# Kernel optimization log

Measured on AMD Instinct MI355X. Metric: run time of the kernel, lower is better.

## Reference

```python
import jax, jax.numpy as jnp
import numpy as np

VOCAB = 50257
EXTRA = 64          # static over-approximation of num_oovs
SEQ = 1024
T_DEC = 100
E = 128
H = 160             # encoder hidden per direction; decoder hidden = 2H = 320
UNK = 3
START = 0
NEG = -1e9


def lstm_cell(x, h, c, wih, whh, bih, bhh):
    # torch gate order: i, f, g, o
    g = x @ wih.T + h @ whh.T + bih + bhh
    i, f, gg, o = jnp.split(g, 4, axis=-1)
    c = jax.nn.sigmoid(f) * c + jax.nn.sigmoid(i) * jnp.tanh(gg)
    h = jax.nn.sigmoid(o) * jnp.tanh(c)
    return h, c


def run_lstm(xs, wih, whh, bih, bhh, hdim):
    def step(carry, x):
        h, c = carry
        h, c = lstm_cell(x, h, c, wih, whh, bih, bhh)
        return (h, c), h
    init = (jnp.zeros((hdim,), xs.dtype), jnp.zeros((hdim,), xs.dtype))
    (hf, _), hs = jax.lax.scan(step, init, xs)
    return hs, hf


def setup_inputs() -> dict:
    key = jax.random.key(0)
    ks = jax.random.split(key, 20)
    rn = lambda k, shape, s: (jax.random.normal(k, shape, dtype=jnp.float32) * s)
    inp = {
        'input_ids': jax.random.randint(ks[0], (SEQ,), 0, VOCAB + EXTRA),
        'embedding': rn(ks[1], (VOCAB, E), 0.1),
        'enc_wih_f': rn(ks[2], (4 * H, E), 0.08),
        'enc_whh_f': rn(ks[3], (4 * H, H), 0.08),
        'enc_bih_f': rn(ks[4], (4 * H,), 0.05),
        'enc_bhh_f': rn(ks[5], (4 * H,), 0.05),
        'enc_wih_b': rn(ks[6], (4 * H, E), 0.08),
        'enc_whh_b': rn(ks[7], (4 * H, H), 0.08),
        'enc_bih_b': rn(ks[8], (4 * H,), 0.05),
        'enc_bhh_b': rn(ks[9], (4 * H,), 0.05),
        'dec_wih': rn(ks[10], (8 * H, E), 0.08),
        'dec_whh': rn(ks[11], (8 * H, 2 * H), 0.08),
        'dec_bih': rn(ks[12], (8 * H,), 0.05),
        'dec_bhh': rn(ks[13], (8 * H,), 0.05),
        'enc_attn_proj': rn(ks[14], (2 * H, 2 * H), 0.02),
        'dec_attn_proj': rn(ks[15], (2 * H, 2 * H), 0.02),
        'vocab_proj': rn(ks[16], (E, 6 * H), 0.05),
        'out_bias': rn(ks[17], (VOCAB,), 0.01),
        'switch_w': rn(ks[18], (1, 6 * H), 0.05),
        'switch_b': rn(ks[19], (1,), 0.05),
    }
    return inp


def reference(input_ids, embedding, enc_wih_f, enc_whh_f, enc_bih_f, enc_bhh_f,
              enc_wih_b, enc_whh_b, enc_bih_b, enc_bhh_b,
              dec_wih, dec_whh, dec_bih, dec_bhh,
              enc_attn_proj, dec_attn_proj, vocab_proj, out_bias,
              switch_w, switch_b):
    ids_in = jnp.where(input_ids >= VOCAB, UNK, input_ids)
    emb = embedding[ids_in]                               # [S, E]

    # bidirectional encoder LSTM
    h_fwd, hfin_f = run_lstm(emb, enc_wih_f, enc_whh_f, enc_bih_f, enc_bhh_f, H)
    h_bwd_rev, hfin_b = run_lstm(emb[::-1], enc_wih_b, enc_whh_b, enc_bih_b, enc_bhh_b, H)
    enc_h = jnp.concatenate([h_fwd, h_bwd_rev[::-1]], axis=-1)   # [S, 2H]

    # step-invariant vocab projection: tanh(W_emb @ vocab_proj) -> [V, 6H]
    out_proj = jnp.tanh(embedding @ vocab_proj)

    # precompute projected encoder states for attention: [S, 2H]
    enc_proj_h = enc_h @ enc_attn_proj.T

    h0 = jnp.concatenate([hfin_f, hfin_b])                # [2H]
    c0 = jnp.zeros((2 * H,), enc_h.dtype)
    dec_buf0 = jnp.zeros((T_DEC, 2 * H), enc_h.dtype)
    cum0 = jnp.zeros((SEQ,), enc_h.dtype)
    tok0 = jnp.asarray(START, dtype=input_ids.dtype)
    t_range = jnp.arange(T_DEC)

    def step(carry, t):
        h, c, cum, dec_buf, tok = carry
        x = embedding[jnp.where(tok >= VOCAB, UNK, tok)]
        h, c = lstm_cell(x, h, c, dec_wih, dec_whh, dec_bih, dec_bhh)

        # intra-temporal encoder attention
        scores = enc_proj_h @ h                           # [S] = h @ W_e @ enc_h.T
        cum_safe = jnp.where(t == 0, 1.0, cum)
        temporal = jnp.where(t == 0, scores, jnp.exp(scores) / cum_safe)
        attn = jax.nn.softmax(temporal)
        enc_ctx = attn @ enc_h                            # [2H]

        # intra-decoder attention over previous decoder hidden states
        dscores = (h @ dec_attn_proj) @ dec_buf.T         # [T_DEC]
        dmask = t_range < t
        dattn = jax.nn.softmax(jnp.where(dmask, dscores, NEG))
        dec_ctx = jnp.where(t == 0, jnp.zeros_like(h), dattn @ dec_buf)

        concat = jnp.concatenate([h, enc_ctx, dec_ctx])   # [6H]
        vocab_dist = jax.nn.softmax(out_proj @ concat + out_bias)  # [V]
        p_copy = jax.nn.sigmoid(jnp.dot(switch_w[0], concat) + switch_b[0])
        gen = jnp.pad((1.0 - p_copy) * vocab_dist, (0, EXTRA))     # [V+EXTRA]
        final = gen.at[input_ids].add(p_copy * attn)      # pointer scatter-add

        cum = cum + scores
        dec_buf = dec_buf.at[t].set(h)
        tok = jnp.argmax(final).astype(input_ids.dtype)   # greedy decode
        return (h, c, cum, dec_buf, tok), final

    _, finals = jax.lax.scan(step, (h0, c0, cum0, dec_buf0, tok0), t_range)
    return finals                                         # [T_DEC, V+EXTRA]
```

## Files before the change

kernel.cpp:

```cpp
#include <hip/hip_runtime.h>
#include <cstdint>

#define VOCAB 50257
#define VTOT  50321
#define TDEC  100
#define UNK   3
#define NBLK  256
#define NTHR  512
#define VPB   256
#define VPAD  50304

static const size_t OFF_EMB    = 0;
static const size_t OFF_WIHT_F = 131072;
static const size_t OFF_WIHT_B = 212992;
static const size_t OFF_WTE    = 294912;
static const size_t OFF_XG     = 397312;
static const size_t OFF_ENCH   = 1708032;
static const size_t OFF_EPH    = 2035712;
static const size_t OFF_DECBUF = 2363392;
static const size_t OFF_GATES  = 2395392;
static const size_t OFF_HPAR   = 2396672;
static const size_t OFF_CPAR   = 2399232;
static const size_t OFF_DCTX   = 2404352;
static const size_t OFF_H0     = 2404672;
static const size_t OFF_TEMP   = 2404992;
static const size_t OFF_ATTN   = 2406016;
static const size_t OFF_PMS    = 2407040;
static const size_t OFF_BM     = 2407552;
static const size_t OFF_BS     = 2407808;
static const size_t OFF_AVAL   = 2408064;
static const size_t OFF_AIDX   = 2408320;
static const size_t OFF_BAR    = 2408576;
static const size_t OFF_SKEY   = 2408640;
static const size_t OFF_SPOS   = 2409664;
static const size_t OFF_BSTART = 2410688;
static const size_t OFF_WT     = 2411008;

__device__ __forceinline__ float sigmf(float x) { return 1.f / (1.f + expf(-x)); }

__device__ __forceinline__ float wsum64(float x) {
#pragma unroll
  for (int m = 1; m < 64; m <<= 1) x += __shfl_xor(x, m, 64);
  return x;
}

__device__ __forceinline__ unsigned short bf16r(float x) {
  uint32_t b = __float_as_uint(x);
  uint32_t r = (b + 0x7fffu + ((b >> 16) & 1u)) >> 16;
  return (unsigned short)r;
}

__device__ __forceinline__ float cload(const float* p) {
  return __hip_atomic_load((float*)p, __ATOMIC_RELAXED, __HIP_MEMORY_SCOPE_AGENT);
}
__device__ __forceinline__ void cstore(float* p, float v) {
  __hip_atomic_store(p, v, __ATOMIC_RELAXED, __HIP_MEMORY_SCOPE_AGENT);
}
__device__ __forceinline__ int cloadi(const int* p) {
  return __hip_atomic_load((int*)p, __ATOMIC_RELAXED, __HIP_MEMORY_SCOPE_AGENT);
}
__device__ __forceinline__ void cstorei(int* p, int v) {
  __hip_atomic_store(p, v, __ATOMIC_RELAXED, __HIP_MEMORY_SCOPE_AGENT);
}

__device__ __forceinline__ void gridbar(float* ws) {
  int* bar = (int*)(ws + OFF_BAR);
  __syncthreads();
  if (threadIdx.x == 0) {
    asm volatile("s_waitcnt vmcnt(0) lgkmcnt(0)" ::: "memory");
    int g = __hip_atomic_load(&bar[32], __ATOMIC_RELAXED, __HIP_MEMORY_SCOPE_AGENT);
    int old = __hip_atomic_fetch_add(&bar[0], 1, __ATOMIC_RELAXED, __HIP_MEMORY_SCOPE_AGENT);
    if (old == NBLK - 1) {
      __hip_atomic_store(&bar[0], 0, __ATOMIC_RELAXED, __HIP_MEMORY_SCOPE_AGENT);
      __hip_atomic_store(&bar[32], g + 1, __ATOMIC_RELAXED, __HIP_MEMORY_SCOPE_AGENT);
    } else {
      while (__hip_atomic_load(&bar[32], __ATOMIC_RELAXED, __HIP_MEMORY_SCOPE_AGENT) == g)
        __builtin_amdgcn_s_sleep(2);
    }
  }
  __syncthreads();
}

__global__ __launch_bounds__(256) void k_setup(float* __restrict__ ws, const int* __restrict__ ids,
                                               const float* __restrict__ embt, const float* __restrict__ ewf,
                                               const float* __restrict__ ewb, const float* __restrict__ eap) {
  int idx = blockIdx.x * 256 + threadIdx.x;
  if (idx < 131072) {
    int tt = idx >> 7, e = idx & 127;
    int id = ids[tt]; if (id >= VOCAB) id = UNK;
    ws[OFF_EMB + idx] = embt[(size_t)id * 128 + e];
  } else if (idx < 212992) {
    int i = idx - 131072;
    int k = i / 640, g = i - (i / 640) * 640;
    ws[OFF_WIHT_F + i] = ewf[(size_t)g * 128 + k];
  } else if (idx < 294912) {
    int i = idx - 212992;
    int k = i / 640, g = i - (i / 640) * 640;
    ws[OFF_WIHT_B + i] = ewb[(size_t)g * 128 + k];
  } else if (idx < 397312) {
    int i = idx - 294912;
    int k = i / 320, j = i - (i / 320) * 320;
    ws[OFF_WTE + i] = eap[(size_t)j * 320 + k];
  }
}

__global__ __launch_bounds__(256) void k_xg(float* __restrict__ ws,
                                            const float* __restrict__ bif, const float* __restrict__ bhf,
                                            const float* __restrict__ bib, const float* __restrict__ bhb) {
  int idx = blockIdx.x * 256 + threadIdx.x;
  int d = idx / 655360;
  int r = idx - d * 655360;
  int tt = r / 640, g = r - (r / 640) * 640;
  const float* wT = ws + (d ? OFF_WIHT_B : OFF_WIHT_F);
  const float* er = ws + OFF_EMB + (size_t)(d ? (1023 - tt) : tt) * 128;
  float acc = d ? (bib[g] + bhb[g]) : (bif[g] + bhf[g]);
#pragma unroll 4
  for (int k = 0; k < 128; ++k) acc += er[k] * wT[(size_t)k * 640 + g];
  ws[OFF_XG + idx] = acc;
}

__global__ __launch_bounds__(256) void k_outproj(const float* __restrict__ embt, const float* __restrict__ vp,
                                                 float* __restrict__ ws) {
  __shared__ float As[64][128];
  __shared__ float Bs[128][64];
  __shared__ unsigned T[32][64];
  const int tid = threadIdx.x;
  const int v0 = blockIdx.x * 64, n0 = blockIdx.y * 64;
  for (int c = 0; c < 32; ++c) {
    int idx = c * 256 + tid;
    int m = idx >> 7, k = idx & 127;
    int v = v0 + m;
    As[m][k] = (v < VOCAB) ? embt[(size_t)v * 128 + k] : 0.f;
    int k2 = idx >> 6, n = idx & 63;
    Bs[k2][n] = vp[(size_t)k2 * 960 + n0 + n];
  }
  __syncthreads();
  const int mi = tid >> 4, ni = tid & 15;
  float acc[4][4] = {};
  for (int k = 0; k < 128; ++k) {
    float a0 = As[mi * 4 + 0][k], a1 = As[mi * 4 + 1][k], a2 = As[mi * 4 + 2][k], a3 = As[mi * 4 + 3][k];
    float4 b = *(const float4*)&Bs[k][ni * 4];
    acc[0][0] += a0 * b.x; acc[0][1] += a0 * b.y; acc[0][2] += a0 * b.z; acc[0][3] += a0 * b.w;
    acc[1][0] += a1 * b.x; acc[1][1] += a1 * b.y; acc[1][2] += a1 * b.z; acc[1][3] += a1 * b.w;
    acc[2][0] += a2 * b.x; acc[2][1] += a2 * b.y; acc[2][2] += a2 * b.z; acc[2][3] += a2 * b.w;
    acc[3][0] += a3 * b.x; acc[3][1] += a3 * b.y; acc[3][2] += a3 * b.z; acc[3][3] += a3 * b.w;
  }
#pragma unroll
  for (int i = 0; i < 4; ++i) {
    unsigned p0 = (unsigned)bf16r(tanhf(acc[i][0])) | ((unsigned)bf16r(tanhf(acc[i][1])) << 16);
    unsigned p1 = (unsigned)bf16r(tanhf(acc[i][2])) | ((unsigned)bf16r(tanhf(acc[i][3])) << 16);
    T[2 * ni][mi * 4 + i] = p0;
    T[2 * ni + 1][mi * 4 + i] = p1;
  }
  __syncthreads();
  unsigned* WT = (unsigned*)(ws + OFF_WT);
  const int kbase = n0 >> 1;
#pragma unroll
  for (int r = 0; r < 8; ++r) {
    int idx = r * 256 + tid;
    int fp = idx >> 6, col = idx & 63;
    int v = v0 + col;
    if (v < VOCAB) WT[(size_t)(kbase + fp) * VPAD + v] = T[fp][col];
  }
}

__global__ __launch_bounds__(512) void k_encoder(float* __restrict__ ws, const float* __restrict__ whh_f,
                                                 const float* __restrict__ whh_b) {
  const int dir = blockIdx.x;
  const int tid = threadIdx.x;
  const float* whh = dir ? whh_b : whh_f;
  const float* xg = ws + OFF_XG + (size_t)dir * 655360;
  __shared__ float hbuf[160];
  __shared__ float part[4][640];
  const int q = tid & 127, kg = tid >> 7, ks = kg * 40;
  float w[5][40];
#pragma unroll
  for (int j = 0; j < 5; ++j)
#pragma unroll
    for (int i = 0; i < 40; ++i)
      w[j][i] = whh[(size_t)(5 * q + j) * 160 + ks + i];
  float cst = 0.f;
  if (tid < 160) hbuf[tid] = 0.f;
  __syncthreads();
  for (int t = 0; t < 1024; ++t) {
    float acc[5] = {0.f, 0.f, 0.f, 0.f, 0.f};
#pragma unroll
    for (int i4 = 0; i4 < 10; ++i4) {
      float4 h4 = *(const float4*)&hbuf[ks + i4 * 4];
#pragma unroll
      for (int j = 0; j < 5; ++j)
        acc[j] += w[j][i4 * 4 + 0] * h4.x + w[j][i4 * 4 + 1] * h4.y + w[j][i4 * 4 + 2] * h4.z + w[j][i4 * 4 + 3] * h4.w;
    }
#pragma unroll
    for (int j = 0; j < 5; ++j) part[kg][5 * q + j] = acc[j];
    __syncthreads();
    if (tid < 160) {
      float gi = xg[(size_t)t * 640 + tid];
      float gf = xg[(size_t)t * 640 + 160 + tid];
      float gg = xg[(size_t)t * 640 + 320 + tid];
      float go = xg[(size_t)t * 640 + 480 + tid];
#pragma unroll
      for (int k2 = 0; k2 < 4; ++k2) {
        gi += part[k2][tid]; gf += part[k2][160 + tid];
        gg += part[k2][320 + tid]; go += part[k2][480 + tid];
      }
      cst = sigmf(gf) * cst + sigmf(gi) * tanhf(gg);
      float hn = sigmf(go) * tanhf(cst);
      hbuf[tid] = hn;
      int trow = dir ? (1023 - t) : t;
      ws[OFF_ENCH + (size_t)trow * 320 + dir * 160 + tid] = hn;
    }
    __syncthreads();
  }
  if (tid < 160) ws[OFF_H0 + dir * 160 + tid] = hbuf[tid];
}

__global__ __launch_bounds__(256) void k_encproj(float* __restrict__ ws) {
  int idx = blockIdx.x * 256 + threadIdx.x;
  int s = idx / 320, j = idx - (idx / 320) * 320;
  const float* er = ws + OFF_ENCH + (size_t)s * 320;
  const float* wt = ws + OFF_WTE;
  float acc = 0.f;
#pragma unroll 4
  for (int k = 0; k < 320; ++k) acc += er[k] * wt[(size_t)k * 320 + j];
  ws[OFF_EPH + idx] = acc;
}

__global__ __launch_bounds__(512) void k_sort(float* __restrict__ ws, const int* __restrict__ ids) {
  __shared__ int sk[1024], sp[1024];
  const int tid = threadIdx.x;
  for (int j = tid; j < 1024; j += 512) { sk[j] = ids[j]; sp[j] = j; }
  __syncthreads();
  for (int k = 2; k <= 1024; k <<= 1)
    for (int j = k >> 1; j > 0; j >>= 1) {
      for (int i = tid; i < 1024; i += 512) {
        int ixj = i ^ j;
        if (ixj > i) {
          bool up = ((i & k) == 0);
          int a = sk[i], b2 = sk[ixj];
          if (up ? (a > b2) : (a < b2)) {
            sk[i] = b2; sk[ixj] = a;
            int pa = sp[i]; sp[i] = sp[ixj]; sp[ixj] = pa;
          }
        }
      }
      __syncthreads();
    }
  int* BST = (int*)(ws + OFF_BSTART);
  int* SK = (int*)(ws + OFF_SKEY);
  int* SP = (int*)(ws + OFF_SPOS);
  for (int j = tid; j < 1024; j += 512) {
    SK[j] = sk[j]; SP[j] = sp[j];
    int o1 = sk[j] / VPB;
    int o0 = (j == 0) ? -1 : (sk[j - 1] / VPB);
    for (int o = o0 + 1; o <= o1; ++o) BST[o] = j;
  }
  if (tid == 0) {
    int olast = sk[1023] / VPB;
    for (int o = olast + 1; o <= NBLK; ++o) BST[o] = 1024;
    int* bar = (int*)(ws + OFF_BAR);
    bar[0] = 0; bar[32] = 0;
  }
}

__global__ __launch_bounds__(512) void k_decode(float* __restrict__ ws, float* __restrict__ out,
    const float* __restrict__ embt,
    const float* __restrict__ dwih, const float* __restrict__ dwhh,
    const float* __restrict__ dbih, const float* __restrict__ dbhh,
    const float* __restrict__ dap, const float* __restrict__ sw,
    const float* __restrict__ sb, const float* __restrict__ ob) {
  const int b = blockIdx.x, tid = threadIdx.x;
  const int l = tid & 63, w = tid >> 6;
  __shared__ __align__(16) float hL[320];
  __shared__ float cL[320];
  __shared__ __align__(16) float concatL[960];
  __shared__ float logitsL[VPB];
  __shared__ float tauL[4], cumL[4];
  __shared__ float redA[512], redB[512];
  __shared__ int   redI[512];
  __shared__ float attnL[64], dsL[128], daL[128], hpL[320];
  __shared__ float pcS;

  const int vrow = b * VPB + (int)tid;
  const bool myrow = (tid < VPB) && (vrow < VOCAB);
  const unsigned* WT = (const unsigned*)(ws + OFF_WT);

  if (tid < 320) { hL[tid] = ws[OFF_H0 + tid]; cL[tid] = 0.f; }
  if (tid < 4) cumL[tid] = 0.f;
  __syncthreads();

  for (int t = 0; t < TDEC; ++t) {
    int token = 0;
    if (t > 0) {
      float av = -1e30f; int ai = 0;
      if (tid < 256) { av = cload(&ws[OFF_AVAL + tid]); ai = cloadi(((const int*)(ws + OFF_AIDX)) + tid); }
      redA[tid] = av; redI[tid] = ai;
      __syncthreads();
      for (int off = 256; off > 0; off >>= 1) {
        if (tid < off) {
          float v2 = redA[tid + off]; int i2 = redI[tid + off];
          if (v2 > redA[tid] || (v2 == redA[tid] && i2 < redI[tid])) { redA[tid] = v2; redI[tid] = i2; }
        }
        __syncthreads();
      }
      token = redI[0];
    }
    int tokm = (token >= VOCAB) ? UNK : token;
    if (w < 5) {
      const int r = 5 * b + w;
      float acc = dwih[(size_t)r * 128 + l] * embt[(size_t)tokm * 128 + l]
                + dwih[(size_t)r * 128 + 64 + l] * embt[(size_t)tokm * 128 + 64 + l];
#pragma unroll
      for (int c = 0; c < 5; ++c) acc += dwhh[(size_t)r * 320 + c * 64 + l] * hL[c * 64 + l];
      acc = wsum64(acc);
      if (l == 0) cstore(&ws[OFF_GATES + r], acc + dbih[r] + dbhh[r]);
    }
    gridbar(ws);

    if (tid < 320) {
      float gi = cload(&ws[OFF_GATES + tid]);
      float gf = cload(&ws[OFF_GATES + 320 + tid]);
      float gg = cload(&ws[OFF_GATES + 640 + tid]);
      float go = cload(&ws[OFF_GATES + 960 + tid]);
      float c = sigmf(gf) * cL[tid] + sigmf(gi) * tanhf(gg);
      cL[tid] = c;
      float hn = sigmf(go) * tanhf(c);
      hL[tid] = hn;
      if (b == 16) ws[OFF_DECBUF + (size_t)t * 320 + tid] = hn;
    }
    __syncthreads();
    if (w < 4) {
      const int srow = 4 * b + w;
      const float* er = ws + OFF_EPH + (size_t)srow * 320;
      float acc = 0.f;
#pragma unroll
      for (int c = 0; c < 5; ++c) acc += er[c * 64 + l] * hL[c * 64 + l];
      acc = wsum64(acc);
      float tau = (t == 0) ? acc : expf(acc) / cumL[w];
      if (l == 0) {
        tauL[w] = tau;
        cstore(&ws[OFF_TEMP + srow], tau);
        cumL[w] += acc;
      }
    }
    if (b < 8 && tid < 320) {
      float acc = 0.f;
#pragma unroll 8
      for (int ii = 0; ii < 40; ++ii) {
        int i = b * 40 + ii;
        acc += hL[i] * dap[(size_t)i * 320 + tid];
      }
      cstore(&ws[OFF_HPAR + b * 320 + tid], acc);
    }
    __syncthreads();
    if (tid == 0) {
      float m4 = fmaxf(fmaxf(tauL[0], tauL[1]), fmaxf(tauL[2], tauL[3]));
      float s4 = expf(tauL[0] - m4) + expf(tauL[1] - m4) + expf(tauL[2] - m4) + expf(tauL[3] - m4);
      cstore(&ws[OFF_PMS + 2 * b], m4);
      cstore(&ws[OFF_PMS + 2 * b + 1], s4);
    }
    gridbar(ws);

    if (b < 16) {
      float m = -1e30f, s = 0.f;
      if (tid < 256) { m = cload(&ws[OFF_PMS + 2 * tid]); s = cload(&ws[OFF_PMS + 2 * tid + 1]); }
      redA[tid] = m; redB[tid] = s;
      __syncthreads();
      for (int off = 256; off > 0; off >>= 1) {
        if (tid < off) {
          float m1 = redA[tid], m2 = redA[tid + off];
          float mx = fmaxf(m1, m2);
          redB[tid] = redB[tid] * expf(m1 - mx) + redB[tid + off] * expf(m2 - mx);
          redA[tid] = mx;
        }
        __syncthreads();
      }
      const float M = redA[0], S = redB[0];
      __syncthreads();
      if (tid < 64) {
        float a = expf(cload(&ws[OFF_TEMP + 64 * b + tid]) - M) / S;
        attnL[tid] = a;
        cstore(&ws[OFF_ATTN + 64 * b + tid], a);
      }
      __syncthreads();
      if (tid < 320) {
        float acc = 0.f;
        const float* eh = ws + OFF_ENCH + (size_t)(64 * b) * 320 + tid;
#pragma unroll 4
        for (int k2 = 0; k2 < 64; ++k2) acc += attnL[k2] * eh[(size_t)k2 * 320];
        cstore(&ws[OFF_CPAR + b * 320 + tid], acc);
      }
    } else if (b == 16) {
      if (tid < 320) {
        float a = 0.f;
#pragma unroll
        for (int q = 0; q < 8; ++q) a += cload(&ws[OFF_HPAR + q * 320 + tid]);
        hpL[tid] = a;
      }
      __syncthreads();
      float hpv[5];
#pragma unroll
      for (int c = 0; c < 5; ++c) hpv[c] = hpL[c * 64 + l];
#pragma unroll
      for (int k2 = 0; k2 < 13; ++k2) {
        int tp = w + 8 * k2;
        if (tp < t) {
          float acc = 0.f;
#pragma unroll
          for (int c = 0; c < 5; ++c) acc += hpv[c] * ws[OFF_DECBUF + (size_t)tp * 320 + c * 64 + l];
          acc = wsum64(acc);
          if (l == 0) dsL[tp] = acc;
        }
      }
      __syncthreads();
      float dv = -1e30f;
      if (tid < 128) { dv = (tid < t) ? dsL[tid] : -1e30f; redA[tid] = dv; }
      __syncthreads();
      for (int off = 64; off > 0; off >>= 1) { if (tid < off) redA[tid] = fmaxf(redA[tid], redA[tid + off]); __syncthreads(); }
      float dmx = redA[0];
      __syncthreads();
      float de = (tid < 128) ? expf(dv - dmx) : 0.f;
      if (tid < 128) redA[tid] = de;
      __syncthreads();
      for (int off = 64; off > 0; off >>= 1) { if (tid < off) redA[tid] += redA[tid + off]; __syncthreads(); }
      float dS = redA[0];
      __syncthreads();
      if (tid < 128) daL[tid] = de / dS;
      __syncthreads();
      if (tid < 320) {
        float acc = 0.f;
        for (int tp = 0; tp < t; ++tp) acc += daL[tp] * ws[OFF_DECBUF + (size_t)tp * 320 + tid];
        cstore(&ws[OFF_DCTX + tid], (t == 0) ? 0.f : acc);
      }
    }
    float ga0 = 0.f, ga1 = 0.f, ga2 = 0.f, ga3 = 0.f;
    if (myrow) {
      const unsigned* wp = WT + vrow;
#pragma unroll 8
      for (int k = 0; k < 160; ++k) {
        unsigned u = wp[(size_t)k * VPAD];
        float2 cv = *(const float2*)&hL[2 * k];
        ga0 += __uint_as_float(u << 16) * cv.x;
        ga1 += __uint_as_float(u & 0xffff0000u) * cv.y;
      }
    }
    gridbar(ws);

    if (tid < 320) {
      float e = 0.f;
#pragma unroll
      for (int g2 = 0; g2 < 16; ++g2) e += cload(&ws[OFF_CPAR + g2 * 320 + tid]);
      concatL[tid] = hL[tid];
      concatL[320 + tid] = e;
      concatL[640 + tid] = cload(&ws[OFF_DCTX + tid]);
    }
    __syncthreads();
    if (w == 0) {
      float acc = 0.f;
#pragma unroll
      for (int c = 0; c < 15; ++c) acc += sw[c * 64 + l] * concatL[c * 64 + l];
      acc = wsum64(acc);
      if (l == 0) pcS = 1.f / (1.f + expf(-(acc + sb[0])));
    }
    if (myrow) {
      const unsigned* wp = WT + vrow;
#pragma unroll 8
      for (int k = 160; k < 480; ++k) {
        unsigned u = wp[(size_t)k * VPAD];
        float2 cv = *(const float2*)&concatL[2 * k];
        ga2 += __uint_as_float(u << 16) * cv.x;
        ga3 += __uint_as_float(u & 0xffff0000u) * cv.y;
      }
    }
    if (tid < VPB) logitsL[tid] = myrow ? (ga0 + ga1 + ga2 + ga3 + ob[vrow]) : -1e30f;
    __syncthreads();
    {
      float m = -1e30f, s = 0.f;
      if (tid < VPB) { float lv = logitsL[tid]; if (lv > -1e29f) { m = lv; s = 1.f; } }
      redA[tid] = m; redB[tid] = s;
      __syncthreads();
      for (int off = 256; off > 0; off >>= 1) {
        if (tid < off) {
          float m1 = redA[tid], m2 = redA[tid + off];
          float mx = fmaxf(m1, m2);
          redB[tid] = redB[tid] * expf(m1 - mx) + redB[tid + off] * expf(m2 - mx);
          redA[tid] = mx;
        }
        __syncthreads();
      }
      if (tid == 0) { cstore(&ws[OFF_BM + b], redA[0]); cstore(&ws[OFF_BS + b], redB[0]); }
    }
    gridbar(ws);

    {
      float m = -1e30f, s = 0.f;
      if (tid < 256) { m = cload(&ws[OFF_BM + tid]); s = cload(&ws[OFF_BS + tid]); }
      redA[tid] = m; redB[tid] = s;
      __syncthreads();
      for (int off = 256; off > 0; off >>= 1) {
        if (tid < off) {
          float m1 = redA[tid], m2 = redA[tid + off];
          float mx = fmaxf(m1, m2);
          redB[tid] = redB[tid] * expf(m1 - mx) + redB[tid + off] * expf(m2 - mx);
          redA[tid] = mx;
        }
        __syncthreads();
      }
      const float M = redA[0], Sg = redB[0];
      const float pc = pcS;
      const float scale = (1.f - pc) / Sg;
      __syncthreads();
      const int* BST = (const int*)(ws + OFF_BSTART);
      const int* SK = (const int*)(ws + OFF_SKEY);
      const int* SP = (const int*)(ws + OFF_SPOS);
      int v = b * VPB + (int)tid;
      bool act = (tid < VPB) && (v < VTOT);
      float val = -1e30f;
      if (act) {
        val = (v < VOCAB) ? scale * expf(logitsL[tid] - M) : 0.f;
        int jb = BST[b], je = BST[b + 1];
        for (int j = jb; j < je; ++j)
          if (SK[j] == v) val += pc * cload(&ws[OFF_ATTN + SP[j]]);
        out[(size_t)t * VTOT + v] = val;
      }
      redA[tid] = act ? val : -1e30f; redI[tid] = v;
      __syncthreads();
      for (int off = 256; off > 0; off >>= 1) {
        if (tid < off) {
          float v2 = redA[tid + off]; int i2 = redI[tid + off];
          if (v2 > redA[tid] || (v2 == redA[tid] && i2 < redI[tid])) { redA[tid] = v2; redI[tid] = i2; }
        }
        __syncthreads();
      }
      if (tid == 0) { cstore(&ws[OFF_AVAL + b], redA[0]); cstorei(((int*)(ws + OFF_AIDX)) + b, redI[0]); }
    }
    gridbar(ws);
  }
}

extern "C" void kernel_launch(void* const* d_in, const int* in_sizes, int n_in,
                              void* d_out, int out_size, void* d_ws, size_t ws_size,
                              hipStream_t stream) {
  const int*   ids  = (const int*)d_in[0];
  const float* embt = (const float*)d_in[1];
  const float* ewf  = (const float*)d_in[2];
  const float* ehf  = (const float*)d_in[3];
  const float* ebif = (const float*)d_in[4];
  const float* ebhf = (const float*)d_in[5];
  const float* ewb  = (const float*)d_in[6];
  const float* ehb  = (const float*)d_in[7];
  const float* ebib = (const float*)d_in[8];
  const float* ebhb = (const float*)d_in[9];
  const float* dwih = (const float*)d_in[10];
  const float* dwhh = (const float*)d_in[11];
  const float* dbih = (const float*)d_in[12];
  const float* dbhh = (const float*)d_in[13];
  const float* eap  = (const float*)d_in[14];
  const float* dap  = (const float*)d_in[15];
  const float* vp   = (const float*)d_in[16];
  const float* ob   = (const float*)d_in[17];
  const float* sw   = (const float*)d_in[18];
  const float* sb   = (const float*)d_in[19];
  float* out = (float*)d_out;
  float* ws  = (float*)d_ws;

  k_setup<<<1558, 256, 0, stream>>>(ws, ids, embt, ewf, ewb, eap);
  k_xg<<<5120, 256, 0, stream>>>(ws, ebif, ebhf, ebib, ebhb);
  k_outproj<<<dim3(786, 15), 256, 0, stream>>>(embt, vp, ws);
  k_encoder<<<2, 512, 0, stream>>>(ws, ehf, ehb);
  k_encproj<<<1280, 256, 0, stream>>>(ws);
  k_sort<<<1, 512, 0, stream>>>(ws, ids);
  k_decode<<<NBLK, NTHR, 0, stream>>>(ws, out, embt, dwih, dwhh, dbih, dbhh, dap, sw, sb, ob);
}
```

Measured before the change: 8.833 ms.

## Re-tile bf16 vocab weights per block with uint4 loads and split K across halves

```diff
diff --git a/kernel.cpp b/kernel.cpp
--- a/kernel.cpp
+++ b/kernel.cpp
@@ -7,34 +7,36 @@
 #define UNK   3
 #define NBLK  256
 #define NTHR  512
-#define VPB   256
-#define VPAD  50304
-
+#define VB0   17
+#define NVB   197
+#define K4N   120
+
+static const size_t OFF_WT     = 0;
 static const size_t OFF_EMB    = 0;
 static const size_t OFF_WIHT_F = 131072;
 static const size_t OFF_WIHT_B = 212992;
 static const size_t OFF_WTE    = 294912;
 static const size_t OFF_XG     = 397312;
-static const size_t OFF_ENCH   = 1708032;
-static const size_t OFF_EPH    = 2035712;
-static const size_t OFF_DECBUF = 2363392;
-static const size_t OFF_GATES  = 2395392;
-static const size_t OFF_HPAR   = 2396672;
-static const size_t OFF_CPAR   = 2399232;
-static const size_t OFF_DCTX   = 2404352;
-static const size_t OFF_H0     = 2404672;
-static const size_t OFF_TEMP   = 2404992;
-static const size_t OFF_ATTN   = 2406016;
-static const size_t OFF_PMS    = 2407040;
-static const size_t OFF_BM     = 2407552;
-static const size_t OFF_BS     = 2407808;
-static const size_t OFF_AVAL   = 2408064;
-static const size_t OFF_AIDX   = 2408320;
-static const size_t OFF_BAR    = 2408576;
-static const size_t OFF_SKEY   = 2408640;
-static const size_t OFF_SPOS   = 2409664;
-static const size_t OFF_BSTART = 2410688;
-static const size_t OFF_WT     = 2411008;
+static const size_t OFF_ENCH   = 24207360;
+static const size_t OFF_EPH    = 24535040;
+static const size_t OFF_DECBUF = 24862720;
+static const size_t OFF_GATES  = 24894720;
+static const size_t OFF_HPAR   = 24896000;
+static const size_t OFF_CPAR   = 24898560;
+static const size_t OFF_DCTX   = 24903680;
+static const size_t OFF_H0     = 24904000;
+static const size_t OFF_TEMP   = 24904320;
+static const size_t OFF_ATTN   = 24905344;
+static const size_t OFF_PMS    = 24906368;
+static const size_t OFF_BM     = 24906880;
+static const size_t OFF_BS     = 24907136;
+static const size_t OFF_AVAL   = 24907392;
+static const size_t OFF_AIDX   = 24907648;
+static const size_t OFF_PC     = 24907904;
+static const size_t OFF_BAR    = 24907968;
+static const size_t OFF_SKEY   = 24908032;
+static const size_t OFF_SPOS   = 24909056;
+static const size_t OFF_BSTART = 24910080;
 
 __device__ __forceinline__ float sigmf(float x) { return 1.f / (1.f + expf(-x)); }
 
@@ -49,6 +51,8 @@
   uint32_t r = (b + 0x7fffu + ((b >> 16) & 1u)) >> 16;
   return (unsigned short)r;
 }
+__device__ __forceinline__ float bflo(unsigned u) { return __uint_as_float(u << 16); }
+__device__ __forceinline__ float bfhi(unsigned u) { return __uint_as_float(u & 0xffff0000u); }
 
 __device__ __forceinline__ float cload(const float* p) {
   return __hip_atomic_load((float*)p, __ATOMIC_RELAXED, __HIP_MEMORY_SCOPE_AGENT);
@@ -119,6 +123,68 @@
   ws[OFF_XG + idx] = acc;
 }
 
+__global__ __launch_bounds__(512) void k_encoder(float* __restrict__ ws, const float* __restrict__ whh_f,
+                                                 const float* __restrict__ whh_b) {
+  const int dir = blockIdx.x;
+  const int tid = threadIdx.x;
+  const float* whh = dir ? whh_b : whh_f;
+  const float* xg = ws + OFF_XG + (size_t)dir * 655360;
+  __shared__ float hbuf[160];
+  __shared__ float part[4][640];
+  const int q = tid & 127, kg = tid >> 7, ks = kg * 40;
+  float w[5][40];
+#pragma unroll
+  for (int j = 0; j < 5; ++j)
+#pragma unroll
+    for (int i = 0; i < 40; ++i)
+      w[j][i] = whh[(size_t)(5 * q + j) * 160 + ks + i];
+  float cst = 0.f;
+  if (tid < 160) hbuf[tid] = 0.f;
+  __syncthreads();
+  for (int t = 0; t < 1024; ++t) {
+    float acc[5] = {0.f, 0.f, 0.f, 0.f, 0.f};
+#pragma unroll
+    for (int i4 = 0; i4 < 10; ++i4) {
+      float4 h4 = *(const float4*)&hbuf[ks + i4 * 4];
+#pragma unroll
+      for (int j = 0; j < 5; ++j)
+        acc[j] += w[j][i4 * 4 + 0] * h4.x + w[j][i4 * 4 + 1] * h4.y + w[j][i4 * 4 + 2] * h4.z + w[j][i4 * 4 + 3] * h4.w;
+    }
+#pragma unroll
+    for (int j = 0; j < 5; ++j) part[kg][5 * q + j] = acc[j];
+    __syncthreads();
+    if (tid < 160) {
+      float gi = xg[(size_t)t * 640 + tid];
+      float gf = xg[(size_t)t * 640 + 160 + tid];
+      float gg = xg[(size_t)t * 640 + 320 + tid];
+      float go = xg[(size_t)t * 640 + 480 + tid];
+#pragma unroll
+      for (int k2 = 0; k2 < 4; ++k2) {
+        gi += part[k2][tid]; gf += part[k2][160 + tid];
+        gg += part[k2][320 + tid]; go += part[k2][480 + tid];
+      }
+      cst = sigmf(gf) * cst + sigmf(gi) * tanhf(gg);
+      float hn = sigmf(go) * tanhf(cst);
+      hbuf[tid] = hn;
+      int trow = dir ? (1023 - t) : t;
+      ws[OFF_ENCH + (size_t)trow * 320 + dir * 160 + tid] = hn;
+    }
+    __syncthreads();
+  }
+  if (tid < 160) ws[OFF_H0 + dir * 160 + tid] = hbuf[tid];
+}
+
+__global__ __launch_bounds__(256) void k_encproj(float* __restrict__ ws) {
+  int idx = blockIdx.x * 256 + threadIdx.x;
+  int s = idx / 320, j = idx - (idx / 320) * 320;
+  const float* er = ws + OFF_ENCH + (size_t)s * 320;
+  const float* wt = ws + OFF_WTE;
+  float acc = 0.f;
+#pragma unroll 4
+  for (int k = 0; k < 320; ++k) acc += er[k] * wt[(size_t)k * 320 + j];
+  ws[OFF_EPH + idx] = acc;
+}
+
 __global__ __launch_bounds__(256) void k_outproj(const float* __restrict__ embt, const float* __restrict__ vp,
                                                  float* __restrict__ ws) {
   __shared__ float As[64][128];
@@ -153,77 +219,21 @@
     T[2 * ni + 1][mi * 4 + i] = p1;
   }
   __syncthreads();
-  unsigned* WT = (unsigned*)(ws + OFF_WT);
-  const int kbase = n0 >> 1;
-#pragma unroll
-  for (int r = 0; r < 8; ++r) {
-    int idx = r * 256 + tid;
-    int fp = idx >> 6, col = idx & 63;
-    int v = v0 + col;
-    if (v < VOCAB) WT[(size_t)(kbase + fp) * VPAD + v] = T[fp][col];
-  }
-}
-
-__global__ __launch_bounds__(512) void k_encoder(float* __restrict__ ws, const float* __restrict__ whh_f,
-                                                 const float* __restrict__ whh_b) {
-  const int dir = blockIdx.x;
-  const int tid = threadIdx.x;
-  const float* whh = dir ? whh_b : whh_f;
-  const float* xg = ws + OFF_XG + (size_t)dir * 655360;
-  __shared__ float hbuf[160];
-  __shared__ float part[4][640];
-  const int q = tid & 127, kg = tid >> 7, ks = kg * 40;
-  float w[5][40];
-#pragma unroll
-  for (int j = 0; j < 5; ++j)
-#pragma unroll
-    for (int i = 0; i < 40; ++i)
-      w[j][i] = whh[(size_t)(5 * q + j) * 160 + ks + i];
-  float cst = 0.f;
-  if (tid < 160) hbuf[tid] = 0.f;
-  __syncthreads();
-  for (int t = 0; t < 1024; ++t) {
-    float acc[5] = {0.f, 0.f, 0.f, 0.f, 0.f};
-#pragma unroll
-    for (int i4 = 0; i4 < 10; ++i4) {
-      float4 h4 = *(const float4*)&hbuf[ks + i4 * 4];
-#pragma unroll
-      for (int j = 0; j < 5; ++j)
-        acc[j] += w[j][i4 * 4 + 0] * h4.x + w[j][i4 * 4 + 1] * h4.y + w[j][i4 * 4 + 2] * h4.z + w[j][i4 * 4 + 3] * h4.w;
-    }
-#pragma unroll
-    for (int j = 0; j < 5; ++j) part[kg][5 * q + j] = acc[j];
-    __syncthreads();
-    if (tid < 160) {
-      float gi = xg[(size_t)t * 640 + tid];
-      float gf = xg[(size_t)t * 640 + 160 + tid];
-      float gg = xg[(size_t)t * 640 + 320 + tid];
-      float go = xg[(size_t)t * 640 + 480 + tid];
-#pragma unroll
-      for (int k2 = 0; k2 < 4; ++k2) {
-        gi += part[k2][tid]; gf += part[k2][160 + tid];
-        gg += part[k2][320 + tid]; go += part[k2][480 + tid];
-      }
-      cst = sigmf(gf) * cst + sigmf(gi) * tanhf(gg);
-      float hn = sigmf(go) * tanhf(cst);
-      hbuf[tid] = hn;
-      int trow = dir ? (1023 - t) : t;
-      ws[OFF_ENCH + (size_t)trow * 320 + dir * 160 + tid] = hn;
-    }
-    __syncthreads();
-  }
-  if (tid < 160) ws[OFF_H0 + dir * 160 + tid] = hbuf[tid];
-}
-
-__global__ __launch_bounds__(256) void k_encproj(float* __restrict__ ws) {
-  int idx = blockIdx.x * 256 + threadIdx.x;
-  int s = idx / 320, j = idx - (idx / 320) * 320;
-  const float* er = ws + OFF_ENCH + (size_t)s * 320;
-  const float* wt = ws + OFF_WTE;
-  float acc = 0.f;
-#pragma unroll 4
-  for (int k = 0; k < 320; ++k) acc += er[k] * wt[(size_t)k * 320 + j];
-  ws[OFF_EPH + idx] = acc;
+  uint4* WT4 = (uint4*)(ws + OFF_WT);
+  const int vb = blockIdx.x >> 2;
+  const int rb = (blockIdx.x & 3) * 64;
+  const int k4b = n0 >> 3;
+#pragma unroll
+  for (int i = 0; i < 2; ++i) {
+    int flat = i * 256 + tid;
+    int k4l = flat >> 6, col = flat & 63;
+    uint4 u;
+    u.x = T[4 * k4l + 0][col];
+    u.y = T[4 * k4l + 1][col];
+    u.z = T[4 * k4l + 2][col];
+    u.w = T[4 * k4l + 3][col];
+    WT4[(size_t)vb * (K4N * 256) + (size_t)(k4b + k4l) * 256 + rb + col] = u;
+  }
 }
 
 __global__ __launch_bounds__(512) void k_sort(float* __restrict__ ws, const int* __restrict__ ids) {
@@ -251,13 +261,19 @@
   int* SP = (int*)(ws + OFF_SPOS);
   for (int j = tid; j < 1024; j += 512) {
     SK[j] = sk[j]; SP[j] = sp[j];
-    int o1 = sk[j] / VPB;
-    int o0 = (j == 0) ? -1 : (sk[j - 1] / VPB);
+    int o1 = sk[j] >> 8;
+    int o0 = (j == 0) ? -1 : (sk[j - 1] >> 8);
     for (int o = o0 + 1; o <= o1; ++o) BST[o] = j;
   }
+  if (tid < 256) {
+    ws[OFF_AVAL + tid] = -1e30f;
+    ((int*)(ws + OFF_AIDX))[tid] = 0;
+    ws[OFF_BM + tid] = -1e30f;
+    ws[OFF_BS + tid] = 0.f;
+  }
   if (tid == 0) {
-    int olast = sk[1023] / VPB;
-    for (int o = olast + 1; o <= NBLK; ++o) BST[o] = 1024;
+    int olast = sk[1023] >> 8;
+    for (int o = olast + 1; o <= NVB; ++o) BST[o] = 1024;
     int* bar = (int*)(ws + OFF_BAR);
     bar[0] = 0; bar[32] = 0;
   }
@@ -271,19 +287,22 @@
     const float* __restrict__ sb, const float* __restrict__ ob) {
   const int b = blockIdx.x, tid = threadIdx.x;
   const int l = tid & 63, w = tid >> 6;
+  const int rl = tid & 255, half = tid >> 8;
+  const int vb = b - VB0;
+  const bool isv = (vb >= 0) && (vb < NVB);
+  const int vrow = isv ? (vb * 256 + rl) : 0;
+  const bool myrow = isv && (vrow < VOCAB);
+  const uint4* WTb = ((const uint4*)(ws + OFF_WT)) + (size_t)(isv ? vb : 0) * (K4N * 256) + rl;
+
   __shared__ __align__(16) float hL[320];
   __shared__ float cL[320];
   __shared__ __align__(16) float concatL[960];
-  __shared__ float logitsL[VPB];
+  __shared__ float logitsL[256];
+  __shared__ float p0L[256], p1L[256];
   __shared__ float tauL[4], cumL[4];
   __shared__ float redA[512], redB[512];
   __shared__ int   redI[512];
   __shared__ float attnL[64], dsL[128], daL[128], hpL[320];
-  __shared__ float pcS;
-
-  const int vrow = b * VPB + (int)tid;
-  const bool myrow = (tid < VPB) && (vrow < VOCAB);
-  const unsigned* WT = (const unsigned*)(ws + OFF_WT);
 
   if (tid < 320) { hL[tid] = ws[OFF_H0 + tid]; cL[tid] = 0.f; }
   if (tid < 4) cumL[tid] = 0.f;
@@ -361,6 +380,7 @@
     }
     gridbar(ws);
 
+    float ga0 = 0.f, ga1 = 0.f;
     if (b < 16) {
       float m = -1e30f, s = 0.f;
       if (tid < 256) { m = cload(&ws[OFF_PMS + 2 * tid]); s = cload(&ws[OFF_PMS + 2 * tid + 1]); }
@@ -432,51 +452,73 @@
         for (int tp = 0; tp < t; ++tp) acc += daL[tp] * ws[OFF_DECBUF + (size_t)tp * 320 + tid];
         cstore(&ws[OFF_DCTX + tid], (t == 0) ? 0.f : acc);
       }
-    }
-    float ga0 = 0.f, ga1 = 0.f, ga2 = 0.f, ga3 = 0.f;
-    if (myrow) {
-      const unsigned* wp = WT + vrow;
-#pragma unroll 8
-      for (int k = 0; k < 160; ++k) {
-        unsigned u = wp[(size_t)k * VPAD];
-        float2 cv = *(const float2*)&hL[2 * k];
-        ga0 += __uint_as_float(u << 16) * cv.x;
-        ga1 += __uint_as_float(u & 0xffff0000u) * cv.y;
+    } else if (isv) {
+      const int c0 = half ? 20 : 0;
+#pragma unroll 10
+      for (int k4 = c0; k4 < c0 + 20; ++k4) {
+        uint4 u = WTb[(size_t)k4 * 256];
+        float4 fa = *(const float4*)&hL[8 * k4];
+        float4 fb = *(const float4*)&hL[8 * k4 + 4];
+        ga0 += bflo(u.x) * fa.x + bflo(u.y) * fa.z + bflo(u.z) * fb.x + bflo(u.w) * fb.z;
+        ga1 += bfhi(u.x) * fa.y + bfhi(u.y) * fa.w + bfhi(u.z) * fb.y + bfhi(u.w) * fb.w;
       }
     }
     gridbar(ws);
 
-    if (tid < 320) {
-      float e = 0.f;
-#pragma unroll
-      for (int g2 = 0; g2 < 16; ++g2) e += cload(&ws[OFF_CPAR + g2 * 320 + tid]);
-      concatL[tid] = hL[tid];
-      concatL[320 + tid] = e;
-      concatL[640 + tid] = cload(&ws[OFF_DCTX + tid]);
-    }
-    __syncthreads();
-    if (w == 0) {
+    if (isv || b == 0) {
+      if (tid < 320) {
+        float e = 0.f;
+#pragma unroll
+        for (int g2 = 0; g2 < 16; ++g2) e += cload(&ws[OFF_CPAR + g2 * 320 + tid]);
+        concatL[tid] = hL[tid];
+        concatL[320 + tid] = e;
+        concatL[640 + tid] = cload(&ws[OFF_DCTX + tid]);
+      }
+    }
+    __syncthreads();
+    if (b == 0 && w == 0) {
       float acc = 0.f;
 #pragma unroll
       for (int c = 0; c < 15; ++c) acc += sw[c * 64 + l] * concatL[c * 64 + l];
       acc = wsum64(acc);
-      if (l == 0) pcS = 1.f / (1.f + expf(-(acc + sb[0])));
-    }
-    if (myrow) {
-      const unsigned* wp = WT + vrow;
+      if (l == 0) cstore(&ws[OFF_PC], 1.f / (1.f + expf(-(acc + sb[0]))));
+    }
+    if (isv) {
+      const int d0 = half ? 80 : 40;
 #pragma unroll 8
-      for (int k = 160; k < 480; ++k) {
-        unsigned u = wp[(size_t)k * VPAD];
-        float2 cv = *(const float2*)&concatL[2 * k];
-        ga2 += __uint_as_float(u << 16) * cv.x;
-        ga3 += __uint_as_float(u & 0xffff0000u) * cv.y;
-      }
-    }
-    if (tid < VPB) logitsL[tid] = myrow ? (ga0 + ga1 + ga2 + ga3 + ob[vrow]) : -1e30f;
-    __syncthreads();
-    {
+      for (int k4 = d0; k4 < d0 + 40; ++k4) {
+        uint4 u = WTb[(size_t)k4 * 256];
+        float4 fa = *(const float4*)&concatL[8 * k4];
+        float4 fb = *(const float4*)&concatL[8 * k4 + 4];
+        ga0 += bflo(u.x) * fa.x + bflo(u.y) * fa.z + bflo(u.z) * fb.x + bflo(u.w) * fb.z;
+        ga1 += bfhi(u.x) * fa.y + bfhi(u.y) * fa.w + bfhi(u.z) * fb.y + bfhi(u.w) * fb.w;
+      }
+      if (half) p1L[rl] = ga0 + ga1; else p0L[rl] = ga0 + ga1;
+    }
+    __syncthreads();
+    float lm = -1e30f, ls = 0.f;
+    if (isv && tid < 256) {
+      float lv = myrow ? (p0L[tid] + p1L[tid] + ob[vrow]) : -1e30f;
+      logitsL[tid] = lv;
+      if (lv > -1e29f) { lm = lv; ls = 1.f; }
+    }
+    redA[tid] = lm; redB[tid] = ls;
+    __syncthreads();
+    for (int off = 256; off > 0; off >>= 1) {
+      if (tid < off) {
+        float m1 = redA[tid], m2 = redA[tid + off];
+        float mx = fmaxf(m1, m2);
+        redB[tid] = redB[tid] * expf(m1 - mx) + redB[tid + off] * expf(m2 - mx);
+        redA[tid] = mx;
+      }
+      __syncthreads();
+    }
+    if (isv && tid == 0) { cstore(&ws[OFF_BM + vb], redA[0]); cstore(&ws[OFF_BS + vb], redB[0]); }
+    gridbar(ws);
+
+    if (isv) {
       float m = -1e30f, s = 0.f;
-      if (tid < VPB) { float lv = logitsL[tid]; if (lv > -1e29f) { m = lv; s = 1.f; } }
+      if (tid < 256) { m = cload(&ws[OFF_BM + tid]); s = cload(&ws[OFF_BS + tid]); }
       redA[tid] = m; redB[tid] = s;
       __syncthreads();
       for (int off = 256; off > 0; off >>= 1) {
@@ -488,42 +530,23 @@
         }
         __syncthreads();
       }
-      if (tid == 0) { cstore(&ws[OFF_BM + b], redA[0]); cstore(&ws[OFF_BS + b], redB[0]); }
-    }
-    gridbar(ws);
-
-    {
-      float m = -1e30f, s = 0.f;
-      if (tid < 256) { m = cload(&ws[OFF_BM + tid]); s = cload(&ws[OFF_BS + tid]); }
-      redA[tid] = m; redB[tid] = s;
-      __syncthreads();
-      for (int off = 256; off > 0; off >>= 1) {
-        if (tid < off) {
-          float m1 = redA[tid], m2 = redA[tid + off];
-          float mx = fmaxf(m1, m2);
-          redB[tid] = redB[tid] * expf(m1 - mx) + redB[tid + off] * expf(m2 - mx);
-          redA[tid] = mx;
-        }
-        __syncthreads();
-      }
       const float M = redA[0], Sg = redB[0];
-      const float pc = pcS;
+      const float pc = cload(&ws[OFF_PC]);
       const float scale = (1.f - pc) / Sg;
       __syncthreads();
       const int* BST = (const int*)(ws + OFF_BSTART);
       const int* SK = (const int*)(ws + OFF_SKEY);
       const int* SP = (const int*)(ws + OFF_SPOS);
-      int v = b * VPB + (int)tid;
-      bool act = (tid < VPB) && (v < VTOT);
+      bool act = (tid < 256) && (vrow < VTOT);
       float val = -1e30f;
       if (act) {
-        val = (v < VOCAB) ? scale * expf(logitsL[tid] - M) : 0.f;
-        int jb = BST[b], je = BST[b + 1];
+        val = (vrow < VOCAB) ? scale * expf(logitsL[tid] - M) : 0.f;
+        int jb = BST[vb], je = BST[vb + 1];
         for (int j = jb; j < je; ++j)
-          if (SK[j] == v) val += pc * cload(&ws[OFF_ATTN + SP[j]]);
-        out[(size_t)t * VTOT + v] = val;
-      }
-      redA[tid] = act ? val : -1e30f; redI[tid] = v;
+          if (SK[j] == vrow) val += pc * cload(&ws[OFF_ATTN + SP[j]]);
+        out[(size_t)t * VTOT + vrow] = val;
+      }
+      redA[tid] = act ? val : -1e30f; redI[tid] = vrow;
       __syncthreads();
       for (int off = 256; off > 0; off >>= 1) {
         if (tid < off) {
@@ -566,9 +589,9 @@
 
   k_setup<<<1558, 256, 0, stream>>>(ws, ids, embt, ewf, ewb, eap);
   k_xg<<<5120, 256, 0, stream>>>(ws, ebif, ebhf, ebib, ebhb);
-  k_outproj<<<dim3(786, 15), 256, 0, stream>>>(embt, vp, ws);
   k_encoder<<<2, 512, 0, stream>>>(ws, ehf, ehb);
   k_encproj<<<1280, 256, 0, stream>>>(ws);
+  k_outproj<<<dim3(786, 15), 256, 0, stream>>>(embt, vp, ws);
   k_sort<<<1, 512, 0, stream>>>(ws, ids);
   k_decode<<<NBLK, NTHR, 0, stream>>>(ws, out, embt, dwih, dwhh, dbih, dbhh, dap, sw, sb, ob);
 }
```

New measurement: 8.535 ms. -3.4%, faster.
